# Performance work log

Measured on AMD Instinct MI355X. Metric: run time of the kernel, lower is better.

## Reference

```python
import jax, jax.numpy as jnp
import numpy as np

B, S, DIM, H = 4, 4096, 2048, 16
HD = DIM // H  # head_dim = 128


def setup_inputs() -> dict:
    key = jax.random.key(0)
    ks = jax.random.split(key, 6)
    X = jax.random.normal(ks[0], (B, S, DIM), dtype=jnp.float32)
    freqs_cos = jax.random.uniform(ks[1], (S, HD), dtype=jnp.float32)
    freqs_sin = jax.random.uniform(ks[2], (S, HD), dtype=jnp.float32)
    attention_mask = jnp.ones((B, S), dtype=jnp.int32)
    # Linear weights stored as [in, out] (equivalent to torch W.T); no bias.
    scale = 0.02
    Wq = jax.random.normal(ks[3], (DIM, DIM), dtype=jnp.float32) * scale
    Wk = jax.random.normal(ks[4], (DIM, DIM), dtype=jnp.float32) * scale
    Wv = jax.random.normal(ks[5], (DIM, DIM), dtype=jnp.float32) * scale
    return {"X": X, "freqs_cos": freqs_cos, "freqs_sin": freqs_sin,
            "attention_mask": attention_mask, "Wq": Wq, "Wk": Wk, "Wv": Wv}


def _rotate_half_interleaved(x):
    # x: [B, S, H, D]; pairs along last dim: (x0, x1) -> (-x1, x0), interleaved
    xp = x.reshape(*x.shape[:-1], HD // 2, 2)
    xt = jnp.stack([-xp[..., 1], xp[..., 0]], axis=-1)
    return xt.reshape(x.shape)


def reference(X, freqs_cos, freqs_sin, attention_mask, Wq, Wk, Wv):
    bs, seq_len, _ = X.shape
    # QKV projections (no bias), fused view to [B, S, H, HD]
    Xq = (X @ Wq).reshape(bs, seq_len, H, HD)
    Xk = (X @ Wk).reshape(bs, seq_len, H, HD)
    Xv = (X @ Wv).reshape(bs, seq_len, H, HD)
    # RoPE: broadcast freqs to (1, S, 1, HD)
    cos = freqs_cos[None, :, None, :]
    sin = freqs_sin[None, :, None, :]
    Xq_out = Xq * cos + _rotate_half_interleaved(Xq) * sin
    Xk_out = Xk * cos + _rotate_half_interleaved(Xk) * sin
    return (Xq_out, Xk_out, Xv)
```

## Files before the change

kernel.cpp:

```cpp
#include <hip/hip_runtime.h>
#include <hip/hip_bf16.h>
#include <stdint.h>

#define B_    4
#define S_    4096
#define DIM_  2048
#define H_    16
#define HD_   128
#define M_    (B_ * S_)
#define K_    DIM_
#define N_    (3 * DIM_)

typedef __attribute__((ext_vector_type(8))) short bf16x8;
typedef __attribute__((ext_vector_type(4))) float f32x4;

__global__ void cvt_x_kernel(const float* __restrict__ X,
                             __hip_bfloat16* __restrict__ Xb) {
    size_t i = ((size_t)blockIdx.x * 256 + threadIdx.x) * 8;
    float4 a = *reinterpret_cast<const float4*>(X + i);
    float4 b = *reinterpret_cast<const float4*>(X + i + 4);
    union { __hip_bfloat16 h[8]; uint4 u; } o;
    o.h[0] = __float2bfloat16(a.x);
    o.h[1] = __float2bfloat16(a.y);
    o.h[2] = __float2bfloat16(a.z);
    o.h[3] = __float2bfloat16(a.w);
    o.h[4] = __float2bfloat16(b.x);
    o.h[5] = __float2bfloat16(b.y);
    o.h[6] = __float2bfloat16(b.z);
    o.h[7] = __float2bfloat16(b.w);
    *reinterpret_cast<uint4*>(Xb + i) = o.u;
}

__global__ void cvt_w_kernel(const float* __restrict__ Wq,
                             const float* __restrict__ Wk,
                             const float* __restrict__ Wv,
                             __hip_bfloat16* __restrict__ Wt) {
    __shared__ float tile[32][33];
    int w = blockIdx.z;
    const float* W = (w == 0) ? Wq : (w == 1) ? Wk : Wv;
    int n0 = blockIdx.x * 32;
    int k0 = blockIdx.y * 32;
    int tx = threadIdx.x, ty = threadIdx.y;
#pragma unroll
    for (int r = 0; r < 4; ++r) {
        int k = k0 + ty + r * 8;
        tile[ty + r * 8][tx] = W[(size_t)k * DIM_ + n0 + tx];
    }
    __syncthreads();
#pragma unroll
    for (int r = 0; r < 4; ++r) {
        int n = n0 + ty + r * 8;
        Wt[(size_t)(w * DIM_ + n) * K_ + k0 + tx] =
            __float2bfloat16(tile[tx][ty + r * 8]);
    }
}

#define BM 256
#define BN 256
#define BK 64
#define NT (K_ / BK)
#define NU (NT / 2)

#define BAR()      asm volatile("s_barrier" ::: "memory")
#define LGKM0()    asm volatile("s_waitcnt lgkmcnt(0)" ::: "memory")
#define LGKM8()    asm volatile("s_waitcnt lgkmcnt(8)" ::: "memory")
#define WAIT_VM(n) asm volatile("s_waitcnt vmcnt(" #n ")" ::: "memory")

__global__ __launch_bounds__(512, 1) void gemm_rope_kernel(
    const __hip_bfloat16* __restrict__ Xb,
    const __hip_bfloat16* __restrict__ Wt,
    const float* __restrict__ fcos,
    const float* __restrict__ fsin,
    float* __restrict__ out)
{
    __shared__ __hip_bfloat16 As[2][BM * BK];
    __shared__ __hip_bfloat16 Bs[2][BN * BK];

    const int nbn = N_ / BN;
    int bid = blockIdx.x;
    int cpx = gridDim.x >> 3;
    int swz = (bid & 7) * cpx + (bid >> 3);
    int tm = swz / nbn, tn = swz % nbn;
    int m0 = tm * BM, n0 = tn * BN;

    int tid  = threadIdx.x;
    int lane = tid & 63;
    int w    = tid >> 6;
    int wr   = w >> 2;
    int wc   = w & 3;

    int rl   = lane >> 3;
    int gsw  = ((lane & 7) ^ rl) * 8;
    int lcol = (lane & 7) * 8;

    int fr = lane & 15;
    int fq = lane >> 4;
    int l7 = lane & 7;
    int ce0 = ((0 + fq) ^ l7) * 8;
    int ce1 = ((4 + fq) ^ l7) * 8;

#define STAGE_A(t, bb, r) do {                                                 \
        const __hip_bfloat16* _s = Xb + (size_t)(m0 + (r) * 64 + w * 8 + rl) * K_ \
                                      + (t) * BK + gsw;                        \
        __hip_bfloat16* _d = &As[bb][((r) * 64 + w * 8 + rl) * BK + lcol];     \
        __builtin_amdgcn_global_load_lds(                                      \
            (const __attribute__((address_space(1))) void*)_s,                 \
            (__attribute__((address_space(3))) void*)_d, 16, 0, 0);            \
    } while (0)

#define STAGE_B(t, bb, r) do {                                                 \
        const __hip_bfloat16* _s = Wt + (size_t)(n0 + (r) * 64 + w * 8 + rl) * K_ \
                                      + (t) * BK + gsw;                        \
        __hip_bfloat16* _d = &Bs[bb][((r) * 64 + w * 8 + rl) * BK + lcol];     \
        __builtin_amdgcn_global_load_lds(                                      \
            (const __attribute__((address_space(1))) void*)_s,                 \
            (__attribute__((address_space(3))) void*)_d, 16, 0, 0);            \
    } while (0)

    f32x4  acc[2][2][4][2] = {};
    bf16x8 a[4][2];
    bf16x8 b[2][2][2];

#define LDA(bb, qi) do {                                                       \
        _Pragma("unroll")                                                      \
        for (int i = 0; i < 4; ++i) {                                          \
            int _row = wr * 128 + (qi) * 64 + i * 16 + fr;                     \
            a[i][0] = *reinterpret_cast<const bf16x8*>(&As[bb][_row * BK + ce0]); \
            a[i][1] = *reinterpret_cast<const bf16x8*>(&As[bb][_row * BK + ce1]); \
        }                                                                      \
    } while (0)

#define LDB(bb, qj) do {                                                       \
        _Pragma("unroll")                                                      \
        for (int j = 0; j < 2; ++j) {                                          \
            int _row = wc * 64 + (qj) * 32 + j * 16 + fr;                      \
            b[qj][j][0] = *reinterpret_cast<const bf16x8*>(&Bs[bb][_row * BK + ce0]); \
            b[qj][j][1] = *reinterpret_cast<const bf16x8*>(&Bs[bb][_row * BK + ce1]); \
        }                                                                      \
    } while (0)

#define MFMA_Q(qi, qj) do {                                                    \
        __builtin_amdgcn_s_setprio(1);                                         \
        _Pragma("unroll")                                                      \
        for (int i = 0; i < 4; ++i)                                            \
        _Pragma("unroll")                                                      \
        for (int j = 0; j < 2; ++j) {                                          \
            acc[qi][qj][i][j] = __builtin_amdgcn_mfma_f32_16x16x32_bf16(       \
                a[i][0], b[qj][j][0], acc[qi][qj][i][j], 0, 0, 0);             \
            acc[qi][qj][i][j] = __builtin_amdgcn_mfma_f32_16x16x32_bf16(       \
                a[i][1], b[qj][j][1], acc[qi][qj][i][j], 0, 0, 0);             \
        }                                                                      \
        __builtin_amdgcn_s_setprio(0);                                         \
    } while (0)

#pragma unroll
    for (int r = 0; r < 4; ++r) STAGE_A(0, 0, r);
#pragma unroll
    for (int r = 0; r < 4; ++r) STAGE_B(0, 0, r);
#pragma unroll
    for (int r = 0; r < 4; ++r) STAGE_B(1, 1, r);
    WAIT_VM(4);
    BAR();

    for (int u = 0; u < NU; ++u) {
        int T0 = 2 * u, T1 = 2 * u + 1;
        bool last = (u == NU - 1);
        LDA(0, 0); LDB(0, 0);
        STAGE_A(T1, 1, 0); STAGE_A(T1, 1, 1);
        LGKM8();
        BAR(); LGKM0();
        MFMA_Q(0, 0);
        BAR();
        LDB(0, 1);
        STAGE_A(T1, 1, 2); STAGE_A(T1, 1, 3);
        BAR(); LGKM0();
        MFMA_Q(0, 1);
        BAR();
        LDA(0, 1);
        if (!last) { STAGE_B(T0 + 2, 0, 0); STAGE_B(T0 + 2, 0, 1); }
        BAR(); LGKM0();
        MFMA_Q(1, 0);
        BAR();
        if (!last) { STAGE_A(T0 + 2, 0, 0); STAGE_A(T0 + 2, 0, 1); }
        BAR();
        MFMA_Q(1, 1);
        if (last) { WAIT_VM(0); } else { WAIT_VM(4); }
        BAR();
        LDA(1, 0); LDB(1, 0);
        if (!last) { STAGE_A(T0 + 2, 0, 2); STAGE_A(T0 + 2, 0, 3); }
        LGKM8();
        BAR(); LGKM0();
        MFMA_Q(0, 0);
        BAR();
        LDB(1, 1);
        if (!last) { STAGE_B(T0 + 2, 0, 2); STAGE_B(T0 + 2, 0, 3); }
        BAR(); LGKM0();
        MFMA_Q(0, 1);
        BAR();
        LDA(1, 1);
        if (!last) { STAGE_B(T1 + 2, 1, 0); STAGE_B(T1 + 2, 1, 1); }
        BAR(); LGKM0();
        MFMA_Q(1, 0);
        BAR();
        if (!last) { STAGE_B(T1 + 2, 1, 2); STAGE_B(T1 + 2, 1, 3); }
        BAR();
        MFMA_Q(1, 1);
        if (!last) { WAIT_VM(4); }
        BAR();
    }

#pragma unroll
    for (int qi = 0; qi < 2; ++qi)
#pragma unroll
    for (int i = 0; i < 4; ++i) {
        int mbase = m0 + wr * 128 + qi * 64 + i * 16 + fq * 4;
#pragma unroll
        for (int qj = 0; qj < 2; ++qj)
#pragma unroll
        for (int j = 0; j < 2; ++j) {
            int n = n0 + wc * 64 + qj * 32 + j * 16 + fr;
            int region = n >> 11;
            int cc = n & (DIM_ - 1);
            int d  = cc & (HD_ - 1);
#pragma unroll
            for (int r = 0; r < 4; ++r) {
                int m = mbase + r;
                int s = m & (S_ - 1);
                float g  = acc[qi][qj][i][j][r];
                float gp = __shfl_xor(g, 1, 64);
                float o;
                if (region < 2) {
                    float cv = fcos[s * HD_ + d];
                    float sv = fsin[s * HD_ + d];
                    o = g * cv + ((cc & 1) ? gp * sv : -gp * sv);
                } else {
                    o = g;
                }
                out[(size_t)region * M_ * DIM_ + (size_t)m * DIM_ + cc] = o;
            }
        }
    }
#undef STAGE_A
#undef STAGE_B
#undef LDA
#undef LDB
#undef MFMA_Q
}

extern "C" void kernel_launch(void* const* d_in, const int* in_sizes, int n_in,
                              void* d_out, int out_size, void* d_ws, size_t ws_size,
                              hipStream_t stream) {
    const float* X    = (const float*)d_in[0];
    const float* fcos = (const float*)d_in[1];
    const float* fsin = (const float*)d_in[2];
    const float* Wq   = (const float*)d_in[4];
    const float* Wk   = (const float*)d_in[5];
    const float* Wv   = (const float*)d_in[6];
    float* out = (float*)d_out;

    __hip_bfloat16* Xb  = (__hip_bfloat16*)d_ws;
    __hip_bfloat16* Wtp = Xb + (size_t)M_ * K_;

    {
        int threads = 256;
        int blocks = (M_ * K_) / (threads * 8);
        cvt_x_kernel<<<blocks, threads, 0, stream>>>(X, Xb);
    }
    {
        dim3 grid(DIM_ / 32, DIM_ / 32, 3);
        dim3 block(32, 8);
        cvt_w_kernel<<<grid, block, 0, stream>>>(Wq, Wk, Wv, Wtp);
    }
    {
        int blocks = (M_ / BM) * (N_ / BN);
        gemm_rope_kernel<<<blocks, 512, 0, stream>>>(Xb, Wtp, fcos, fsin, out);
    }
}
```

Baseline: 572.9 us.

## Switch GEMM inner tile from 16x16x32 to 32x32x16 bf16 MFMA

Replaces the 16x16x32 MFMA fragments with 32x32x16 MFMA, reorganizing the LDS read layout (swizzled row/group indexing), accumulator shape, and the epilogue's row/column mapping for the RoPE write-out. The larger MFMA tile needs fewer LDS fragment reads per FLOP and fewer instructions. It also moves the LDS waitcnt after each MFMA block instead of before, so fragment loads can overlap the matrix ops. This risks register pressure and correctness if the swizzle or epilogue mapping is wrong.

```diff
diff --git a/kernel.cpp b/kernel.cpp
--- a/kernel.cpp
+++ b/kernel.cpp
@@ -11,8 +11,8 @@
 #define K_    DIM_
 #define N_    (3 * DIM_)
 
-typedef __attribute__((ext_vector_type(8))) short bf16x8;
-typedef __attribute__((ext_vector_type(4))) float f32x4;
+typedef __attribute__((ext_vector_type(8)))  short bf16x8;
+typedef __attribute__((ext_vector_type(16))) float f32x16;
 
 __global__ void cvt_x_kernel(const float* __restrict__ X,
                              __hip_bfloat16* __restrict__ Xb) {
@@ -63,7 +63,6 @@
 
 #define BAR()      asm volatile("s_barrier" ::: "memory")
 #define LGKM0()    asm volatile("s_waitcnt lgkmcnt(0)" ::: "memory")
-#define LGKM8()    asm volatile("s_waitcnt lgkmcnt(8)" ::: "memory")
 #define WAIT_VM(n) asm volatile("s_waitcnt vmcnt(" #n ")" ::: "memory")
 
 __global__ __launch_bounds__(512, 1) void gemm_rope_kernel(
@@ -93,11 +92,8 @@
     int gsw  = ((lane & 7) ^ rl) * 8;
     int lcol = (lane & 7) * 8;
 
-    int fr = lane & 15;
-    int fq = lane >> 4;
-    int l7 = lane & 7;
-    int ce0 = ((0 + fq) ^ l7) * 8;
-    int ce1 = ((4 + fq) ^ l7) * 8;
+    int l31 = lane & 31;
+    int l1  = lane >> 5;
 
 #define STAGE_A(t, bb, r) do {                                                 \
         const __hip_bfloat16* _s = Xb + (size_t)(m0 + (r) * 64 + w * 8 + rl) * K_ \
@@ -117,39 +113,43 @@
             (__attribute__((address_space(3))) void*)_d, 16, 0, 0);            \
     } while (0)
 
-    f32x4  acc[2][2][4][2] = {};
-    bf16x8 a[4][2];
-    bf16x8 b[2][2][2];
+    f32x16 acc[4][2] = {};
+    bf16x8 a[2][4];
+    bf16x8 b[2][4];
 
 #define LDA(bb, qi) do {                                                       \
         _Pragma("unroll")                                                      \
-        for (int i = 0; i < 4; ++i) {                                          \
-            int _row = wr * 128 + (qi) * 64 + i * 16 + fr;                     \
-            a[i][0] = *reinterpret_cast<const bf16x8*>(&As[bb][_row * BK + ce0]); \
-            a[i][1] = *reinterpret_cast<const bf16x8*>(&As[bb][_row * BK + ce1]); \
+        for (int ii = 0; ii < 2; ++ii) {                                       \
+            int _row = wr * 128 + ((qi) * 2 + ii) * 32 + l31;                  \
+            int _s7  = _row & 7;                                               \
+            _Pragma("unroll")                                                  \
+            for (int kk = 0; kk < 4; ++kk) {                                   \
+                int _g = (kk * 2 + l1) ^ _s7;                                  \
+                a[ii][kk] = *reinterpret_cast<const bf16x8*>(                  \
+                    &As[bb][_row * BK + _g * 8]);                              \
+            }                                                                  \
         }                                                                      \
     } while (0)
 
 #define LDB(bb, qj) do {                                                       \
-        _Pragma("unroll")                                                      \
-        for (int j = 0; j < 2; ++j) {                                          \
-            int _row = wc * 64 + (qj) * 32 + j * 16 + fr;                      \
-            b[qj][j][0] = *reinterpret_cast<const bf16x8*>(&Bs[bb][_row * BK + ce0]); \
-            b[qj][j][1] = *reinterpret_cast<const bf16x8*>(&Bs[bb][_row * BK + ce1]); \
+        int _row = wc * 64 + (qj) * 32 + l31;                                  \
+        int _s7  = _row & 7;                                                   \
+        _Pragma("unroll")                                                      \
+        for (int kk = 0; kk < 4; ++kk) {                                       \
+            int _g = (kk * 2 + l1) ^ _s7;                                      \
+            b[qj][kk] = *reinterpret_cast<const bf16x8*>(                      \
+                &Bs[bb][_row * BK + _g * 8]);                                  \
         }                                                                      \
     } while (0)
 
 #define MFMA_Q(qi, qj) do {                                                    \
         __builtin_amdgcn_s_setprio(1);                                         \
         _Pragma("unroll")                                                      \
-        for (int i = 0; i < 4; ++i)                                            \
-        _Pragma("unroll")                                                      \
-        for (int j = 0; j < 2; ++j) {                                          \
-            acc[qi][qj][i][j] = __builtin_amdgcn_mfma_f32_16x16x32_bf16(       \
-                a[i][0], b[qj][j][0], acc[qi][qj][i][j], 0, 0, 0);             \
-            acc[qi][qj][i][j] = __builtin_amdgcn_mfma_f32_16x16x32_bf16(       \
-                a[i][1], b[qj][j][1], acc[qi][qj][i][j], 0, 0, 0);             \
-        }                                                                      \
+        for (int ii = 0; ii < 2; ++ii)                                         \
+        _Pragma("unroll")                                                      \
+        for (int kk = 0; kk < 4; ++kk)                                         \
+            acc[(qi) * 2 + ii][qj] = __builtin_amdgcn_mfma_f32_32x32x16_bf16(  \
+                a[ii][kk], b[qj][kk], acc[(qi) * 2 + ii][qj], 0, 0, 0);        \
         __builtin_amdgcn_s_setprio(0);                                         \
     } while (0)
 
@@ -167,19 +167,21 @@
         bool last = (u == NU - 1);
         LDA(0, 0); LDB(0, 0);
         STAGE_A(T1, 1, 0); STAGE_A(T1, 1, 1);
-        LGKM8();
-        BAR(); LGKM0();
+        BAR();
         MFMA_Q(0, 0);
+        LGKM0();
         BAR();
         LDB(0, 1);
         STAGE_A(T1, 1, 2); STAGE_A(T1, 1, 3);
-        BAR(); LGKM0();
+        BAR();
         MFMA_Q(0, 1);
+        LGKM0();
         BAR();
         LDA(0, 1);
         if (!last) { STAGE_B(T0 + 2, 0, 0); STAGE_B(T0 + 2, 0, 1); }
-        BAR(); LGKM0();
+        BAR();
         MFMA_Q(1, 0);
+        LGKM0();
         BAR();
         if (!last) { STAGE_A(T0 + 2, 0, 0); STAGE_A(T0 + 2, 0, 1); }
         BAR();
@@ -188,19 +190,21 @@
         BAR();
         LDA(1, 0); LDB(1, 0);
         if (!last) { STAGE_A(T0 + 2, 0, 2); STAGE_A(T0 + 2, 0, 3); }
-        LGKM8();
-        BAR(); LGKM0();
+        BAR();
         MFMA_Q(0, 0);
+        LGKM0();
         BAR();
         LDB(1, 1);
         if (!last) { STAGE_B(T0 + 2, 0, 2); STAGE_B(T0 + 2, 0, 3); }
-        BAR(); LGKM0();
+        BAR();
         MFMA_Q(0, 1);
+        LGKM0();
         BAR();
         LDA(1, 1);
         if (!last) { STAGE_B(T1 + 2, 1, 0); STAGE_B(T1 + 2, 1, 1); }
-        BAR(); LGKM0();
+        BAR();
         MFMA_Q(1, 0);
+        LGKM0();
         BAR();
         if (!last) { STAGE_B(T1 + 2, 1, 2); STAGE_B(T1 + 2, 1, 3); }
         BAR();
@@ -210,34 +214,28 @@
     }
 
 #pragma unroll
-    for (int qi = 0; qi < 2; ++qi)
-#pragma unroll
-    for (int i = 0; i < 4; ++i) {
-        int mbase = m0 + wr * 128 + qi * 64 + i * 16 + fq * 4;
-#pragma unroll
-        for (int qj = 0; qj < 2; ++qj)
-#pragma unroll
-        for (int j = 0; j < 2; ++j) {
-            int n = n0 + wc * 64 + qj * 32 + j * 16 + fr;
-            int region = n >> 11;
-            int cc = n & (DIM_ - 1);
-            int d  = cc & (HD_ - 1);
-#pragma unroll
-            for (int r = 0; r < 4; ++r) {
-                int m = mbase + r;
-                int s = m & (S_ - 1);
-                float g  = acc[qi][qj][i][j][r];
-                float gp = __shfl_xor(g, 1, 64);
-                float o;
-                if (region < 2) {
-                    float cv = fcos[s * HD_ + d];
-                    float sv = fsin[s * HD_ + d];
-                    o = g * cv + ((cc & 1) ? gp * sv : -gp * sv);
-                } else {
-                    o = g;
-                }
-                out[(size_t)region * M_ * DIM_ + (size_t)m * DIM_ + cc] = o;
+    for (int ib = 0; ib < 4; ++ib)
+#pragma unroll
+    for (int jb = 0; jb < 2; ++jb) {
+        int n = n0 + wc * 64 + jb * 32 + l31;
+        int region = n >> 11;
+        int cc = n & (DIM_ - 1);
+        int d  = cc & (HD_ - 1);
+#pragma unroll
+        for (int reg = 0; reg < 16; ++reg) {
+            int m = m0 + wr * 128 + ib * 32 + (reg & 3) + 8 * (reg >> 2) + 4 * l1;
+            int s = m & (S_ - 1);
+            float g  = acc[ib][jb][reg];
+            float gp = __shfl_xor(g, 1, 64);
+            float o;
+            if (region < 2) {
+                float cv = fcos[s * HD_ + d];
+                float sv = fsin[s * HD_ + d];
+                o = g * cv + ((cc & 1) ? gp * sv : -gp * sv);
+            } else {
+                o = g;
             }
+            out[(size_t)region * M_ * DIM_ + (size_t)m * DIM_ + cc] = o;
         }
     }
 #undef STAGE_A
```

After: 674.1 us. +17.7%, slower.
